# Optimization experiments

Measured on AMD Instinct MI355X. Metric: run time of the kernel, lower is better.

The kernel has to match this reference:

```python
import jax, jax.numpy as jnp
import numpy as np

FRACTION = 0.33  # from attn_type='query_selector_0.33'


def setup_inputs() -> dict:
    key = jax.random.key(0)
    k1, k2, k3, k4 = jax.random.split(key, 4)
    B, L, DIM_VAL, DIM_ATTN = 8, 4096, 64, 64
    scale = 1.0 / np.sqrt(DIM_VAL).astype(np.float32)
    x = jax.random.normal(k1, (B, L, DIM_VAL), dtype=jnp.float32)
    Wq = jax.random.normal(k2, (DIM_VAL, DIM_ATTN), dtype=jnp.float32) * scale
    Wk = jax.random.normal(k3, (DIM_VAL, DIM_ATTN), dtype=jnp.float32) * scale
    Wv = jax.random.normal(k4, (DIM_VAL, DIM_VAL), dtype=jnp.float32) * scale
    return {"x": x, "Wq": Wq, "Wk": Wk, "Wv": Wv}


def reference(x, Wq, Wk, Wv):
    # Projections (bias-free Linears)
    Q = jnp.einsum('bld,de->ble', x, Wq)  # [B, L, Da]
    K = jnp.einsum('bld,de->ble', x, Wk)  # [B, L, Da]
    V = jnp.einsum('bld,de->ble', x, Wv)  # [B, L, Dv]

    B, L_Q, Da = Q.shape
    l_Q = int((1.0 - FRACTION) * L_Q)  # static: shapes known at trace time

    # keys.topk(l_Q, dim=1).values -> per-channel top-l_Q along seq; mean over them
    K_top = jax.lax.top_k(jnp.swapaxes(K, 1, 2), l_Q)[0]  # [B, Da, l_Q]
    K_reduce = K_top.mean(axis=-1)                         # [B, Da]

    # score each query against the reduced key; pick top-l_Q queries
    sqk = jnp.einsum('bd,bld->bl', K_reduce, Q)            # [B, L_Q]
    indices = jax.lax.top_k(sqk, l_Q)[1]                   # [B, l_Q] int32

    # gather sampled queries
    Q_sample = jnp.take_along_axis(Q, indices[:, :, None], axis=1)  # [B, l_Q, Da]

    # dense attention for the sampled queries only
    scores = jnp.einsum('bqd,bkd->bqk', Q_sample, K) / jnp.sqrt(jnp.asarray(Da, Q.dtype))
    attn = jax.nn.softmax(scores, axis=-1)                 # [B, l_Q, L]
    out_sel = jnp.einsum('bqk,bkv->bqv', attn, V)          # [B, l_Q, Dv]

    # mean-filled result, scatter attention outputs to selected rows
    mean_values = V.mean(axis=-2)                          # [B, Dv]
    result = jnp.broadcast_to(mean_values[:, None, :], (B, L_Q, V.shape[-1]))
    result = result.at[jnp.arange(B)[:, None], indices].set(out_sel)
    return result
```

## Files before the change

### kernel.cpp

```cpp
#include <hip/hip_runtime.h>
#include <hip/hip_bf16.h>
#include <math.h>

#define BATCH 8
#define SEQ   4096
#define DIM   64
#define LQ    2744
#define QPB   128
#define NQB   22
#define QPAD  2816
#define KS    8
#define L2E   1.4426950408889634f
#define QSC   0.1803368801111204f

typedef _Float16 half8 __attribute__((ext_vector_type(8)));
typedef short    bs8   __attribute__((ext_vector_type(8)));
typedef float    fx16  __attribute__((ext_vector_type(16)));
typedef unsigned short ushort_t;

union UH { uint4 u4; half8 h; };
union UB { unsigned u[4]; uint4 u4; bs8 s; };

__device__ __forceinline__ unsigned pack_bf16(float a, float b) {
    __hip_bfloat162 h = __float22bfloat162_rn(make_float2(a, b));
    union { __hip_bfloat162 h; unsigned u; } cv; cv.h = h; return cv.u;
}

__device__ __forceinline__ unsigned f2sort(float f) {
    unsigned u = __float_as_uint(f);
    return (u & 0x80000000u) ? ~u : (u | 0x80000000u);
}
__device__ __forceinline__ float sort2f(unsigned u) {
    return __uint_as_float((u & 0x80000000u) ? (u & 0x7FFFFFFFu) : ~u);
}

__device__ void radix_select_4096(const unsigned* u, int k, unsigned* hist,
                                  unsigned* wsum, unsigned* res) {
    const int t = threadIdx.x;
    const int lane = t & 63, wv = t >> 6;
    if (t == 0) { res[0] = 0u; res[1] = (unsigned)k; }
    for (int pass = 3; pass >= 0; --pass) {
        const int shift = pass * 8;
        hist[t] = 0u;
        __syncthreads();
        const unsigned pref  = res[0];
        const unsigned kk    = res[1];
        const unsigned hmask = (pass == 3) ? 0u : (0xFFFFFFFFu << (shift + 8));
        for (int i = t; i < 4096; i += 256) {
            unsigned ui = u[i];
            if ((ui & hmask) == pref) atomicAdd(&hist[(ui >> shift) & 255u], 1u);
        }
        __syncthreads();
        const unsigned h = hist[t];
        unsigned s = h;
#pragma unroll
        for (int ofs = 1; ofs < 64; ofs <<= 1) {
            unsigned a = __shfl_down(s, ofs, 64);
            s += (lane + ofs < 64) ? a : 0u;
        }
        if (lane == 0) wsum[wv] = s;
        __syncthreads();
#pragma unroll
        for (int w2 = 0; w2 < 4; ++w2)
            if (w2 > wv) s += wsum[w2];
        if (s >= kk && (s - h) < kk) {
            res[0] = pref | ((unsigned)t << shift);
            res[1] = kk - (s - h);
        }
        __syncthreads();
    }
}

__global__ __launch_bounds__(256) void proj_kernel(
    const float* __restrict__ x,  const float* __restrict__ Wq,
    const float* __restrict__ Wk, const float* __restrict__ Wv,
    float* __restrict__ Q, float* __restrict__ Kt,
    _Float16* __restrict__ Qh, _Float16* __restrict__ Kh,
    ushort_t* __restrict__ Vt, float* __restrict__ pmean) {
    const int rt = blockIdx.x, b = blockIdx.y, t = threadIdx.x;
    __shared__ float4 xs4[64 * 17];
    __shared__ float  red[4][64];
    {
        const float4* xg = (const float4*)(x + ((size_t)b * SEQ + rt * 64) * DIM);
        for (int i = 0; i < 4; ++i) {
            int s = t + 256 * i;
            xs4[(s >> 4) * 17 + (s & 15)] = xg[s];
        }
    }
    __syncthreads();
    const int ch = t & 63, rg = t >> 6;
    float accq[16], acck[16], accv[16];
#pragma unroll
    for (int i = 0; i < 16; ++i) { accq[i] = 0.f; acck[i] = 0.f; accv[i] = 0.f; }
    for (int dc = 0; dc < 4; ++dc) {
        float wq[16], wk[16], wv[16];
#pragma unroll
        for (int dd = 0; dd < 16; ++dd) {
            int d = dc * 16 + dd;
            wq[dd] = Wq[d * 64 + ch]; wk[dd] = Wk[d * 64 + ch]; wv[dd] = Wv[d * 64 + ch];
        }
        for (int r = 0; r < 16; ++r) {
            const int row = rg * 16 + r;
            const float4* xr = &xs4[row * 17 + dc * 4];
            float xv[16];
            float4 a0 = xr[0], a1 = xr[1], a2 = xr[2], a3 = xr[3];
            xv[0]=a0.x; xv[1]=a0.y; xv[2]=a0.z; xv[3]=a0.w;
            xv[4]=a1.x; xv[5]=a1.y; xv[6]=a1.z; xv[7]=a1.w;
            xv[8]=a2.x; xv[9]=a2.y; xv[10]=a2.z; xv[11]=a2.w;
            xv[12]=a3.x; xv[13]=a3.y; xv[14]=a3.z; xv[15]=a3.w;
#pragma unroll
            for (int dd = 0; dd < 16; ++dd) {
                accq[r] = fmaf(xv[dd], wq[dd], accq[r]);
                acck[r] = fmaf(xv[dd], wk[dd], acck[r]);
                accv[r] = fmaf(xv[dd], wv[dd], accv[r]);
            }
        }
    }
    const int rowbase = rt * 64 + rg * 16;
    float sv = 0.f;
#pragma unroll
    for (int r = 0; r < 16; ++r) {
        size_t o = ((size_t)b * SEQ + rowbase + r) * DIM + ch;
        Q[o]  = accq[r];
        Qh[o] = (_Float16)(accq[r] * QSC);
        Kh[o] = (_Float16)acck[r];
        sv += accv[r];
    }
    float4* ktp = (float4*)(Kt + ((size_t)b * 64 + ch) * SEQ + rowbase);
    ktp[0] = make_float4(acck[0], acck[1], acck[2], acck[3]);
    ktp[1] = make_float4(acck[4], acck[5], acck[6], acck[7]);
    ktp[2] = make_float4(acck[8], acck[9], acck[10], acck[11]);
    ktp[3] = make_float4(acck[12], acck[13], acck[14], acck[15]);
    {
        unsigned pk[8];
#pragma unroll
        for (int i = 0; i < 8; ++i) pk[i] = pack_bf16(accv[2*i], accv[2*i+1]);
        uint4* vp = (uint4*)(Vt + ((size_t)(b * 64 + ch)) * SEQ + rowbase);
        vp[0] = make_uint4(pk[0], pk[1], pk[4], pk[5]);
        vp[1] = make_uint4(pk[2], pk[3], pk[6], pk[7]);
    }
    red[rg][ch] = sv;
    __syncthreads();
    if (rg == 0)
        pmean[((size_t)b * 64 + ch) * 64 + rt] =
            red[0][ch] + red[1][ch] + red[2][ch] + red[3][ch];
}

__global__ __launch_bounds__(256) void kmean_kernel(const float* __restrict__ Kt,
                                                    const float* __restrict__ pmean,
                                                    float* __restrict__ Kred,
                                                    float* __restrict__ meanfin) {
    __shared__ unsigned u[4096];
    __shared__ unsigned hist[256];
    __shared__ unsigned wsum[4];
    __shared__ unsigned res[2];
    __shared__ float rsum[4];
    const int bc = blockIdx.x, t = threadIdx.x;
    if (t < 64) {
        float v = pmean[(size_t)bc * 64 + t];
        for (int m = 1; m < 64; m <<= 1) v += __shfl_xor(v, m, 64);
        if (t == 0) meanfin[bc] = v * (1.0f / (float)SEQ);
    }
    const float4* c4 = (const float4*)(Kt + (size_t)bc * SEQ);
    for (int i = t; i < 1024; i += 256) {
        float4 v = c4[i];
        u[i*4+0] = f2sort(v.x); u[i*4+1] = f2sort(v.y);
        u[i*4+2] = f2sort(v.z); u[i*4+3] = f2sort(v.w);
    }
    __syncthreads();
    radix_select_4096(u, LQ, hist, wsum, res);
    const unsigned Tu = res[0];
    const int krem = (int)res[1];
    float loc = 0.f;
    for (int i = t; i < 4096; i += 256)
        if (u[i] > Tu) loc += sort2f(u[i]);
    for (int msk = 1; msk < 64; msk <<= 1) loc += __shfl_xor(loc, msk, 64);
    if ((t & 63) == 0) rsum[t >> 6] = loc;
    __syncthreads();
    if (t == 0) {
        float s = rsum[0] + rsum[1] + rsum[2] + rsum[3] + (float)krem * sort2f(Tu);
        Kred[bc] = s / (float)LQ;
    }
}

__global__ __launch_bounds__(256) void sqk_kernel(const float* __restrict__ Q,
                                                  const float* __restrict__ Kred,
                                                  float* __restrict__ sqk) {
    const int b = blockIdx.y, l = blockIdx.x * 256 + threadIdx.x;
    __shared__ float kr[64];
    if (threadIdx.x < 64) kr[threadIdx.x] = Kred[b * 64 + threadIdx.x];
    __syncthreads();
    const float4* q = (const float4*)(Q + ((size_t)b * SEQ + l) * DIM);
    float s = 0.f;
#pragma unroll
    for (int i = 0; i < 16; ++i) {
        float4 v = q[i];
        s = fmaf(v.x, kr[i*4+0], s); s = fmaf(v.y, kr[i*4+1], s);
        s = fmaf(v.z, kr[i*4+2], s); s = fmaf(v.w, kr[i*4+3], s);
    }
    sqk[b * SEQ + l] = s;
}

__global__ __launch_bounds__(256) void select_kernel(const float* __restrict__ sqk,
                                                     int* __restrict__ sel,
                                                     int* __restrict__ inv) {
    __shared__ unsigned u[4096];
    __shared__ unsigned hist[256];
    __shared__ unsigned wsum[4];
    __shared__ unsigned res[2];
    __shared__ int eq_idx[256];
    __shared__ int cnts[2];
    const int b = blockIdx.x, t = threadIdx.x;
    const float* col = sqk + (size_t)b * SEQ;
    int* invb = inv + (size_t)b * SEQ;
    for (int i = t; i < 4096; i += 256) {
        u[i] = f2sort(col[i]);
        invb[i] = -1;
    }
    if (t < 2) cnts[t] = 0;
    __syncthreads();
    radix_select_4096(u, LQ, hist, wsum, res);
    const unsigned Tu = res[0];
    const int krem = (int)res[1];
    int* selb = sel + b * QPAD;
    for (int i = t; i < 4096; i += 256) {
        unsigned ui = u[i];
        if (ui > Tu) {
            int p = atomicAdd(&cnts[0], 1);
            selb[p] = i;
            invb[i] = p;
        } else if (ui == Tu) {
            int p = atomicAdd(&cnts[1], 1);
            if (p < 256) eq_idx[p] = i;
        }
    }
    __syncthreads();
    if (t == 0) {
        int ng = cnts[0];
        int ne = cnts[1] < 256 ? cnts[1] : 256;
        for (int i = 1; i < ne; ++i) {
            int v = eq_idx[i], j = i - 1;
            while (j >= 0 && eq_idx[j] > v) { eq_idx[j+1] = eq_idx[j]; --j; }
            eq_idx[j+1] = v;
        }
        for (int j = 0; j < krem; ++j) {
            selb[ng + j] = eq_idx[j];
            invb[eq_idx[j]] = ng + j;
        }
    }
    __syncthreads();
    if (t < QPAD - LQ) selb[LQ + t] = selb[LQ - 1];
}

__global__ __launch_bounds__(256, 3) void attn_kernel(
    const ushort_t* __restrict__ Qh, const ushort_t* __restrict__ Kh,
    const ushort_t* __restrict__ Vt, const int* __restrict__ sel,
    float* __restrict__ pl, float* __restrict__ pout) {
    const int lin = blockIdx.x + NQB * (blockIdx.y + KS * blockIdx.z);
    const int ks  = lin & 7;
    const int j8  = lin >> 3;
    const int b   = j8 / NQB;
    const int qt  = j8 % NQB;
    const int t = threadIdx.x, w = t >> 6, lane = t & 63;
    const int col = lane & 31, h = lane >> 5;

    __shared__ ushort_t Ktile[2][32 * 64];
    __shared__ ushort_t Vtile[2][32 * 64];

    half8 qf[4];
    {
        const int q = qt * QPB + w * 32 + col;
        const int row = sel[b * QPAD + q];
        const uint4* qg = (const uint4*)(Qh + ((size_t)b * SEQ + row) * DIM);
#pragma unroll
        for (int m = 0; m < 4; ++m) { UH u; u.u4 = qg[2 * m + h]; qf[m] = u.h; }
    }

    int koff[4], voff[4];
#pragma unroll
    for (int m = 0; m < 4; ++m)
        koff[m] = col * 64 + 8 * ((2 * m + h) ^ (col & 7));
#pragma unroll
    for (int i = 0; i < 4; ++i)
        voff[i] = col * 64 + 8 * ((i * 2 + h) ^ (col & 7));

    fx16 O0, O1;
#pragma unroll
    for (int r = 0; r < 16; ++r) { O0[r] = 0.f; O1[r] = 0.f; }
    float l = 0.f;

    const int srow = t >> 3, sgr = t & 7;
    const int lg = sgr ^ (srow & 7);
    const int vD = lg >> 2, vc = (lg >> 1) & 1, vh = lg & 1;
    const size_t kgbase = ((size_t)b * SEQ + ks * 512 + srow) * DIM + 8 * lg;
    const size_t vgbase = ((size_t)(b * DIM + srow + 32 * vD)) * SEQ
                          + ks * 512 + vc * 16 + vh * 8;

    uint4 kreg = *(const uint4*)(Kh + kgbase);
    uint4 vreg = *(const uint4*)(Vt + vgbase);

    for (int tile = 0; tile < 16; ++tile) {
        const int buf = tile & 1;
        *(uint4*)&Ktile[buf][srow * 64 + sgr * 8] = kreg;
        *(uint4*)&Vtile[buf][srow * 64 + sgr * 8] = vreg;
        __syncthreads();
        if (tile < 15) {
            kreg = *(const uint4*)(Kh + kgbase + (size_t)(tile + 1) * 32 * DIM);
            vreg = *(const uint4*)(Vt + vgbase + (size_t)(tile + 1) * 32);
        }
        fx16 S;
#pragma unroll
        for (int r = 0; r < 16; ++r) S[r] = 0.f;
#pragma unroll
        for (int m = 0; m < 4; ++m) {
            UH kf;
            kf.u4 = *(const uint4*)&Ktile[buf][koff[m]];
            S = __builtin_amdgcn_mfma_f32_32x32x16_f16(kf.h, qf[m], S, 0, 0, 0);
        }
        float p[16];
#pragma unroll
        for (int r = 0; r < 16; ++r) p[r] = exp2f(S[r]);
#pragma unroll
        for (int r = 0; r < 16; ++r) l += p[r];
        UB A0, A1;
#pragma unroll
        for (int v = 0; v < 4; ++v) {
            A0.u[v] = pack_bf16(p[2 * v],     p[2 * v + 1]);
            A1.u[v] = pack_bf16(p[8 + 2 * v], p[8 + 2 * v + 1]);
        }
#pragma unroll
        for (int D = 0; D < 2; ++D) {
            fx16& O = D ? O1 : O0;
#pragma unroll
            for (int c = 0; c < 2; ++c) {
                UB vf;
                vf.u4 = *(const uint4*)&Vtile[buf][voff[D * 2 + c]];
                O = __builtin_amdgcn_mfma_f32_32x32x16_bf16(c ? A1.s : A0.s, vf.s, O, 0, 0, 0);
            }
        }
    }

    l += __shfl_xor(l, 32);

    const int qg0 = qt * QPB + w * 32;
    const size_t base = (size_t)b * QPAD + qg0;
#pragma unroll
    for (int D = 0; D < 2; ++D) {
        const fx16& O = D ? O1 : O0;
#pragma unroll
        for (int r = 0; r < 16; ++r) {
            const int q = (r & 3) + 8 * (r >> 2) + 4 * h;
            atomicAdd(&pout[(base + q) * DIM + D * 32 + col], O[r]);
        }
    }
    if (h == 0) atomicAdd(&pl[base + col], l);
}

__global__ __launch_bounds__(256) void comb_kernel(
    const float* __restrict__ pl, const float* __restrict__ pout,
    const int* __restrict__ inv, const float* __restrict__ meanfin,
    float* __restrict__ out) {
    const int idx = blockIdx.x * 256 + threadIdx.x;
    const int b = idx >> 16;
    const int rc = idx & 65535;
    const int row = rc >> 4, c = rc & 15;
    const int p = inv[b * SEQ + row];
    float4 o;
    if (p >= 0) {
        const size_t s0 = (size_t)b * QPAD + p;
        const float invl = 1.0f / pl[s0];
        float4 a = ((const float4*)(pout + s0 * DIM))[c];
        o = make_float4(a.x * invl, a.y * invl, a.z * invl, a.w * invl);
    } else {
        o = make_float4(meanfin[b * 64 + c * 4 + 0], meanfin[b * 64 + c * 4 + 1],
                        meanfin[b * 64 + c * 4 + 2], meanfin[b * 64 + c * 4 + 3]);
    }
    ((float4*)out)[idx] = o;
}

extern "C" void kernel_launch(void* const* d_in, const int* in_sizes, int n_in,
                              void* d_out, int out_size, void* d_ws, size_t ws_size,
                              hipStream_t stream) {
    const float* x  = (const float*)d_in[0];
    const float* Wq = (const float*)d_in[1];
    const float* Wk = (const float*)d_in[2];
    const float* Wv = (const float*)d_in[3];
    float* out = (float*)d_out;
    char* wsb  = (char*)d_ws;

    float*    Q       = (float*)(wsb);
    _Float16* Qh      = (_Float16*)(wsb + 8388608);
    _Float16* Kh      = (_Float16*)(wsb + 12582912);
    ushort_t* Vt      = (ushort_t*)(wsb + 16777216);
    float*    pmean   = (float*)(wsb + 20971520);
    float*    meanfin = (float*)(wsb + 21102592);
    float*    Kred    = (float*)(wsb + 21104640);
    float*    sqk     = (float*)(wsb + 21106688);
    int*      sel     = (int*)(wsb + 21237760);
    int*      inv     = (int*)(wsb + 21327872);
    float*    Kt      = (float*)(wsb + 21458944);
    float*    pout    = (float*)(wsb + 21458944);
    float*    pl      = (float*)(wsb + 21458944 + 5767168);

    proj_kernel  <<<dim3(64, 8),          256, 0, stream>>>(x, Wq, Wk, Wv, Q, Kt,
                                                            Qh, Kh, Vt, pmean);
    kmean_kernel <<<512,                  256, 0, stream>>>(Kt, pmean, Kred, meanfin);
    sqk_kernel   <<<dim3(16, 8),          256, 0, stream>>>(Q, Kred, sqk);
    select_kernel<<<8,                    256, 0, stream>>>(sqk, sel, inv);
    hipMemsetAsync(pout, 0, 5767168 + 90112, stream);
    attn_kernel  <<<dim3(NQB, KS, BATCH), 256, 0, stream>>>((const ushort_t*)Qh,
                                                            (const ushort_t*)Kh,
                                                            Vt, sel, pl, pout);
    comb_kernel  <<<2048,                 256, 0, stream>>>(pl, pout, inv, meanfin, out);
}
```

Before: 195.5 us.

## Load K/V MFMA fragments directly from global memory and fuse output zeroing into sqk

The attention kernel no longer stages K and V tiles through double-buffered shared memory with block-wide barriers. Each lane now loads its MFMA fragments straight from global memory into registers, with two register sets alternating so the next tile's loads overlap the current tile's compute. The cost is that all four waves fetch the same K/V data separately and the per-lane accesses are less coalesced, so the kernel leans on L1/L2 hits. Separately, the hipMemsetAsync of the partial-output buffers is removed and the zeroing is done inside sqk_kernel, saving one operation on the stream.

```diff
diff --git a/kernel.cpp b/kernel.cpp
--- a/kernel.cpp
+++ b/kernel.cpp
@@ -185,10 +185,16 @@
 
 __global__ __launch_bounds__(256) void sqk_kernel(const float* __restrict__ Q,
                                                   const float* __restrict__ Kred,
-                                                  float* __restrict__ sqk) {
+                                                  float* __restrict__ sqk,
+                                                  float4* __restrict__ pz) {
     const int b = blockIdx.y, l = blockIdx.x * 256 + threadIdx.x;
     __shared__ float kr[64];
     if (threadIdx.x < 64) kr[threadIdx.x] = Kred[b * 64 + threadIdx.x];
+    {
+        const int tid = (blockIdx.y * 16 + blockIdx.x) * 256 + threadIdx.x;
+        const float4 z = make_float4(0.f, 0.f, 0.f, 0.f);
+        for (int i = tid; i < 366080; i += 32768) pz[i] = z;
+    }
     __syncthreads();
     const float4* q = (const float4*)(Q + ((size_t)b * SEQ + l) * DIM);
     float s = 0.f;
@@ -264,9 +270,6 @@
     const int t = threadIdx.x, w = t >> 6, lane = t & 63;
     const int col = lane & 31, h = lane >> 5;
 
-    __shared__ ushort_t Ktile[2][32 * 64];
-    __shared__ ushort_t Vtile[2][32 * 64];
-
     half8 qf[4];
     {
         const int q = qt * QPB + w * 32 + col;
@@ -276,45 +279,28 @@
         for (int m = 0; m < 4; ++m) { UH u; u.u4 = qg[2 * m + h]; qf[m] = u.h; }
     }
 
-    int koff[4], voff[4];
-#pragma unroll
-    for (int m = 0; m < 4; ++m)
-        koff[m] = col * 64 + 8 * ((2 * m + h) ^ (col & 7));
-#pragma unroll
-    for (int i = 0; i < 4; ++i)
-        voff[i] = col * 64 + 8 * ((i * 2 + h) ^ (col & 7));
+    const ushort_t* kb0 = Kh + ((size_t)b * SEQ + ks * 512 + col) * DIM + 8 * h;
+    const ushort_t* vb0 = Vt + ((size_t)b * DIM + col) * SEQ + ks * 512 + 8 * h;
 
     fx16 O0, O1;
 #pragma unroll
     for (int r = 0; r < 16; ++r) { O0[r] = 0.f; O1[r] = 0.f; }
     float l = 0.f;
 
-    const int srow = t >> 3, sgr = t & 7;
-    const int lg = sgr ^ (srow & 7);
-    const int vD = lg >> 2, vc = (lg >> 1) & 1, vh = lg & 1;
-    const size_t kgbase = ((size_t)b * SEQ + ks * 512 + srow) * DIM + 8 * lg;
-    const size_t vgbase = ((size_t)(b * DIM + srow + 32 * vD)) * SEQ
-                          + ks * 512 + vc * 16 + vh * 8;
-
-    uint4 kreg = *(const uint4*)(Kh + kgbase);
-    uint4 vreg = *(const uint4*)(Vt + vgbase);
-
-    for (int tile = 0; tile < 16; ++tile) {
-        const int buf = tile & 1;
-        *(uint4*)&Ktile[buf][srow * 64 + sgr * 8] = kreg;
-        *(uint4*)&Vtile[buf][srow * 64 + sgr * 8] = vreg;
-        __syncthreads();
-        if (tile < 15) {
-            kreg = *(const uint4*)(Kh + kgbase + (size_t)(tile + 1) * 32 * DIM);
-            vreg = *(const uint4*)(Vt + vgbase + (size_t)(tile + 1) * 32);
-        }
+    uint4 ka[4], va[4], kc[4], vc[4];
+#pragma unroll
+    for (int m = 0; m < 4; ++m) ka[m] = *(const uint4*)(kb0 + 16 * m);
+#pragma unroll
+    for (int i = 0; i < 4; ++i)
+        va[i] = *(const uint4*)(vb0 + (size_t)(i >> 1) * 32 * SEQ + (i & 1) * 16);
+
+    auto step = [&](const uint4* kf4, const uint4* vf4) {
         fx16 S;
 #pragma unroll
         for (int r = 0; r < 16; ++r) S[r] = 0.f;
 #pragma unroll
         for (int m = 0; m < 4; ++m) {
-            UH kf;
-            kf.u4 = *(const uint4*)&Ktile[buf][koff[m]];
+            UH kf; kf.u4 = kf4[m];
             S = __builtin_amdgcn_mfma_f32_32x32x16_f16(kf.h, qf[m], S, 0, 0, 0);
         }
         float p[16];
@@ -333,11 +319,34 @@
             fx16& O = D ? O1 : O0;
 #pragma unroll
             for (int c = 0; c < 2; ++c) {
-                UB vf;
-                vf.u4 = *(const uint4*)&Vtile[buf][voff[D * 2 + c]];
-                O = __builtin_amdgcn_mfma_f32_32x32x16_bf16(c ? A1.s : A0.s, vf.s, O, 0, 0, 0);
+                UB vf; vf.u4 = vf4[D * 2 + c];
+                O = __builtin_amdgcn_mfma_f32_32x32x16_bf16(c ? A1.s : A0.s, vf.s,
+                                                            O, 0, 0, 0);
             }
         }
+    };
+
+    for (int tile = 0; tile < 16; tile += 2) {
+        {
+            const ushort_t* kp = kb0 + (size_t)(tile + 1) * 32 * DIM;
+            const ushort_t* vp = vb0 + (tile + 1) * 32;
+#pragma unroll
+            for (int m = 0; m < 4; ++m) kc[m] = *(const uint4*)(kp + 16 * m);
+#pragma unroll
+            for (int i = 0; i < 4; ++i)
+                vc[i] = *(const uint4*)(vp + (size_t)(i >> 1) * 32 * SEQ + (i & 1) * 16);
+        }
+        step(ka, va);
+        if (tile + 2 < 16) {
+            const ushort_t* kp = kb0 + (size_t)(tile + 2) * 32 * DIM;
+            const ushort_t* vp = vb0 + (tile + 2) * 32;
+#pragma unroll
+            for (int m = 0; m < 4; ++m) ka[m] = *(const uint4*)(kp + 16 * m);
+#pragma unroll
+            for (int i = 0; i < 4; ++i)
+                va[i] = *(const uint4*)(vp + (size_t)(i >> 1) * 32 * SEQ + (i & 1) * 16);
+        }
+        step(kc, vc);
     }
 
     l += __shfl_xor(l, 32);
@@ -405,9 +414,9 @@
     proj_kernel  <<<dim3(64, 8),          256, 0, stream>>>(x, Wq, Wk, Wv, Q, Kt,
                                                             Qh, Kh, Vt, pmean);
     kmean_kernel <<<512,                  256, 0, stream>>>(Kt, pmean, Kred, meanfin);
-    sqk_kernel   <<<dim3(16, 8),          256, 0, stream>>>(Q, Kred, sqk);
+    sqk_kernel   <<<dim3(16, 8),          256, 0, stream>>>(Q, Kred, sqk,
+                                                            (float4*)pout);
     select_kernel<<<8,                    256, 0, stream>>>(sqk, sel, inv);
-    hipMemsetAsync(pout, 0, 5767168 + 90112, stream);
     attn_kernel  <<<dim3(NQB, KS, BATCH), 256, 0, stream>>>((const ushort_t*)Qh,
                                                             (const ushort_t*)Kh,
                                                             Vt, sel, pl, pout);
```

New measurement: 236.5 us. 21.0% more time.
